# Kernel optimization log

Measured on AMD Instinct MI355X. Metric: run time of the kernel, lower is better.

Reference implementation:

```python
import jax, jax.numpy as jnp
import numpy as np

N = 50000
E = 1600000
INPUT_DIM = 128
HEADS = 4
OUT_DIM = 32
LRELU_ALPHA = 0.2


def setup_inputs() -> dict:
    key = jax.random.key(0)
    k1, k2, k3, k4, k5 = jax.random.split(key, 5)
    gain = 1.0 / (1.0 + LRELU_ALPHA)
    input_proj = jax.random.normal(k1, (N, INPUT_DIM), dtype=jnp.float32)
    edge_index = jax.random.randint(k2, (2, E), 0, N, dtype=jnp.int64)
    W = jax.random.normal(k3, (INPUT_DIM, HEADS * OUT_DIM), dtype=jnp.float32) * (gain / INPUT_DIM) ** 0.5
    A_left = jax.random.normal(k4, (HEADS, OUT_DIM, 1), dtype=jnp.float32) * (gain / OUT_DIM)
    A_right = jax.random.normal(k5, (HEADS, OUT_DIM, 1), dtype=jnp.float32) * (gain / OUT_DIM)
    return {"input_proj": input_proj, "edge_index": edge_index, "W": W, "A_left": A_left, "A_right": A_right}


def reference(input_proj, edge_index, W, A_left, A_right):
    n = input_proj.shape[0]
    heads, out_dim = A_left.shape[0], A_left.shape[1]
    # Linear projection: [N, heads, out_dim]
    H = (input_proj @ W).reshape(n, heads, out_dim)
    # Per-node attention scores: [N, heads]
    H_s = jnp.einsum('nhd,hd->nh', H, A_left[..., 0])
    H_t = jnp.einsum('nhd,hd->nh', H, A_right[..., 0])
    src = edge_index[0]
    tgt = edge_index[1]
    # Edge scores: leaky_relu(H_s[src] + H_t[tgt]) -> [E, heads]
    e = H_s[src] + H_t[tgt]
    e = jnp.where(e > 0, e, LRELU_ALPHA * e)
    # Segment softmax over neighborhoods keyed by source node (global max shift, as in original)
    e = jnp.exp(e - jnp.max(e))
    denom = jax.ops.segment_sum(e, src, num_segments=n)  # [N, heads]
    alpha = e / (denom[src] + 1e-8)
    # Weighted scatter-add aggregation of target features: [N, heads, out_dim]
    msg = alpha[:, :, None] * H[tgt]
    agg = jax.ops.segment_sum(msg, src, num_segments=n)
    # concat_last=True -> [N, heads*out_dim], then ELU
    res = agg.reshape(n, heads * out_dim)
    return jax.nn.elu(res)
```

## Files before the change

### kernel.cpp

```cpp
#include <hip/hip_runtime.h>
#include <hip/hip_fp16.h>

#define DIM 128
#define HEADS 4
#define ODIM 32
#define LRELU 0.2f
#define PT 4096
#define CAP 9216

typedef unsigned int u32;
typedef unsigned short u16;
typedef unsigned char u8;

typedef __attribute__((ext_vector_type(8))) short bf16x8;
typedef __attribute__((ext_vector_type(4))) float f32x4;

__device__ __forceinline__ u16 f2bf(float f) {
    union { u32 u; float f; } x; x.f = f;
    u32 u = x.u;
    u32 r = u + 0x7FFFu + ((u >> 16) & 1u);
    return (u16)(r >> 16);
}
__device__ __forceinline__ u32 pack_h2(float x, float y) {
    union { __half2 h; u32 u; } c;
    c.h = __floats2half2_rn(x, y);
    return c.u;
}
__device__ __forceinline__ float2 up2(u32 b) {
    union { u32 u; __half2 h; } c; c.u = b;
    return __half22float2(c.h);
}

__device__ __forceinline__ int scan256_excl(int v, int t, int* wsum) {
    int lane = t & 63, w = t >> 6;
    int inc = v;
    #pragma unroll
    for (int ofs = 1; ofs < 64; ofs <<= 1) {
        int x = __shfl_up(inc, ofs);
        if (lane >= ofs) inc += x;
    }
    __syncthreads();
    if (lane == 63) wsum[w] = inc;
    __syncthreads();
    int add = 0;
    #pragma unroll
    for (int j = 0; j < 4; ++j) add += (j < w) ? wsum[j] : 0;
    return inc - v + add;
}

__global__ __launch_bounds__(256) void prep_kernel(
    const float* __restrict__ W, u16* __restrict__ Wt, int* __restrict__ bcur)
{
    __shared__ u16 s[128 * 17];
    const int t = threadIdx.x;
    const int b = blockIdx.x;
    if (b == 0) bcur[t] = t * CAP;
    #pragma unroll
    for (int i = 0; i < 8; ++i) {
        int idx = i * 256 + t;
        int kk = idx >> 7;
        int nn = idx & 127;
        s[nn * 17 + kk] = f2bf(W[(b * 16 + kk) * 128 + nn]);
    }
    __syncthreads();
    #pragma unroll
    for (int i = 0; i < 8; ++i) {
        int idx = i * 256 + t;
        int nn = idx >> 4;
        int kk = idx & 15;
        Wt[nn * 128 + b * 16 + kk] = s[nn * 17 + kk];
    }
}

__device__ __forceinline__ void partition_body(
    char* smem, int bid, const int* __restrict__ ei, int* __restrict__ bcur,
    u32* __restrict__ part, int E, int n)
{
    int (*lcnt4)[256] = (int (*)[256])(smem);
    int (*gcur4)[256] = (int (*)[256])(smem + 4096);
    const int t = threadIdx.x;
    const int wv = t >> 6;
    const int base = bid * PT;
    lcnt4[0][t] = 0; lcnt4[1][t] = 0; lcnt4[2][t] = 0; lcnt4[3][t] = 0;
    __syncthreads();

    int srcv[16], tgtv[16];
    #pragma unroll
    for (int i = 0; i < 16; ++i) {
        int e = base + i * 256 + t;
        srcv[i] = (e < E) ? ei[e] : -1;
    }
    #pragma unroll
    for (int i = 0; i < 16; ++i) {
        int e = base + i * 256 + t;
        tgtv[i] = (e < E) ? ei[E + e] : 0;
    }
    u32 key[16];
    int bkt[16];
    #pragma unroll
    for (int i = 0; i < 16; ++i) {
        bkt[i] = -1;
        key[i] = 0;
        if (srcv[i] >= 0) {
            int src = min(srcv[i], n - 1);
            int tgt = max(0, min(tgtv[i], n - 1));
            bkt[i] = src >> 8;
            key[i] = ((u32)(src & 255) << 17) | (u32)tgt;
        }
    }
    #pragma unroll
    for (int i = 0; i < 16; ++i)
        if (bkt[i] >= 0) atomicAdd(&lcnt4[wv][bkt[i]], 1);
    __syncthreads();
    int c0 = lcnt4[0][t], c1 = lcnt4[1][t], c2 = lcnt4[2][t], c3 = lcnt4[3][t];
    int total = c0 + c1 + c2 + c3;
    int gb = (total > 0) ? atomicAdd(&bcur[t], total) : 0;
    gcur4[0][t] = gb;
    gcur4[1][t] = gb + c0;
    gcur4[2][t] = gb + c0 + c1;
    gcur4[3][t] = gb + c0 + c1 + c2;
    __syncthreads();
    #pragma unroll
    for (int i = 0; i < 16; ++i) {
        if (bkt[i] >= 0) {
            int p = atomicAdd(&gcur4[wv][bkt[i]], 1);
            if (p < (bkt[i] + 1) * CAP) part[p] = key[i];
        }
    }
}

__device__ __forceinline__ void proj_body(
    char* smem, int bid, const float* __restrict__ X, const u16* __restrict__ Wt,
    const float* __restrict__ AL, const float* __restrict__ AR,
    u32* __restrict__ Hb, float* __restrict__ Hs, float* __restrict__ Ht, int n)
{
    float* sH  = (float*)smem;
    float* sAL = (float*)(smem + 33792);
    float* sAR = (float*)(smem + 34304);
    const int t = threadIdx.x;
    if (t < DIM) { sAL[t] = AL[t]; sAR[t] = AR[t]; }
    const int row0 = bid * 64;
    const int w = t >> 6, lane = t & 63;
    const int quad = lane >> 4, nIdx = lane & 15;
    const int m = row0 + w * 16 + nIdx;

    f32x4 acc[8];
    #pragma unroll
    for (int c = 0; c < 8; ++c) acc[c] = (f32x4){0.f, 0.f, 0.f, 0.f};

    #pragma unroll
    for (int kq = 0; kq < 4; ++kq) {
        union { bf16x8 v; u16 e[8]; } a;
        if (m < n) {
            const float* xp = &X[(size_t)m * DIM + kq * 32 + quad * 8];
            float4 x0 = *(const float4*)xp;
            float4 x1 = *(const float4*)(xp + 4);
            a.e[0] = f2bf(x0.x); a.e[1] = f2bf(x0.y);
            a.e[2] = f2bf(x0.z); a.e[3] = f2bf(x0.w);
            a.e[4] = f2bf(x1.x); a.e[5] = f2bf(x1.y);
            a.e[6] = f2bf(x1.z); a.e[7] = f2bf(x1.w);
        } else {
            #pragma unroll
            for (int j = 0; j < 8; ++j) a.e[j] = 0;
        }
        #pragma unroll
        for (int c = 0; c < 8; ++c) {
            bf16x8 b = *(const bf16x8*)&Wt[(c * 16 + nIdx) * DIM + kq * 32 + quad * 8];
            acc[c] = __builtin_amdgcn_mfma_f32_16x16x32_bf16(a.v, b, acc[c], 0, 0, 0);
        }
    }
    #pragma unroll
    for (int c = 0; c < 8; ++c)
        #pragma unroll
        for (int r = 0; r < 4; ++r)
            sH[(w * 16 + quad * 4 + r) * 132 + c * 16 + nIdx] = acc[c][r];
    __syncthreads();

    #pragma unroll
    for (int i = 0; i < 16; ++i) {
        int idx = i * 256 + t;
        int r = idx >> 6, d2 = idx & 63;
        int gr = row0 + r;
        if (gr < n) {
            float2 hv = *(const float2*)&sH[r * 132 + 2 * d2];
            Hb[(size_t)gr * 64 + d2] = pack_h2(hv.x, hv.y);
        }
    }
    {
        int r = t >> 2, h = t & 3;
        float s = 0.f, s2 = 0.f;
        #pragma unroll
        for (int q = 0; q < ODIM; q += 4) {
            float4 hv = *(const float4*)&sH[r * 132 + h * ODIM + q];
            s  += hv.x*sAL[h*ODIM+q] + hv.y*sAL[h*ODIM+q+1] + hv.z*sAL[h*ODIM+q+2] + hv.w*sAL[h*ODIM+q+3];
            s2 += hv.x*sAR[h*ODIM+q] + hv.y*sAR[h*ODIM+q+1] + hv.z*sAR[h*ODIM+q+2] + hv.w*sAR[h*ODIM+q+3];
        }
        int gr = row0 + r;
        if (gr < n) { Hs[gr * HEADS + h] = s; Ht[gr * HEADS + h] = s2; }
    }
}

__global__ __launch_bounds__(256) void fused_pp_kernel(
    const float* __restrict__ X, const u16* __restrict__ Wt,
    const float* __restrict__ AL, const float* __restrict__ AR,
    u32* __restrict__ Hb, float* __restrict__ Hs, float* __restrict__ Ht,
    const int* __restrict__ ei, int* __restrict__ bcur, u32* __restrict__ part,
    int n, int E, int partBlocks)
{
    __shared__ alignas(16) char smem[34816];
    if ((int)blockIdx.x < partBlocks)
        partition_body(smem, blockIdx.x, ei, bcur, part, E, n);
    else
        proj_body(smem, blockIdx.x - partBlocks, X, Wt, AL, AR, Hb, Hs, Ht, n);
}

__global__ __launch_bounds__(256) void csrfill_kernel(
    const u32* __restrict__ part, const int* __restrict__ bcur,
    int* __restrict__ off, int* __restrict__ csr_tgt, int n, int ntiles)
{
    __shared__ u32 skey[CAP];
    __shared__ int lc4[4][128];
    __shared__ int lcur4[4][128];
    __shared__ int wsum[4];
    __shared__ int sBase, sCnt;
    const int blk = blockIdx.x, t = threadIdx.x;
    const int b = blk >> 1, half = blk & 1;
    const int wv = t >> 6;
    int myc = (t < ntiles) ? (bcur[t] - t * CAP) : 0;
    myc = max(0, min(myc, CAP));
    int ex = scan256_excl(myc, t, wsum);
    if (t == b) { sBase = ex; sCnt = myc; }
    if (t < 128) { lc4[0][t] = 0; lc4[1][t] = 0; lc4[2][t] = 0; lc4[3][t] = 0; }
    __syncthreads();
    const int pbase = b * CAP;
    const int base = sBase, cnt = sCnt;
    for (int i = t; i < cnt; i += 1024) {
        u32 k[4];
        #pragma unroll
        for (int u = 0; u < 4; ++u) {
            int idx = i + u * 256;
            k[u] = (idx < cnt) ? part[pbase + idx] : 0xFFFFFFFFu;
        }
        #pragma unroll
        for (int u = 0; u < 4; ++u) {
            int idx = i + u * 256;
            if (idx < cnt) skey[idx] = k[u];
            int n8 = (int)(k[u] >> 17);
            if ((n8 >> 7) == half) atomicAdd(&lc4[wv][n8 & 127], 1);
        }
    }
    __syncthreads();
    int c0 = 0, c1 = 0, c2 = 0, c3 = 0, total = 0;
    if (t < 128) {
        c0 = lc4[0][t]; c1 = lc4[1][t]; c2 = lc4[2][t]; c3 = lc4[3][t];
        total = c0 + c1 + c2 + c3;
    }
    int ex2 = scan256_excl(total, t, wsum);
    int halfTot = wsum[0] + wsum[1];
    int myBase = base + (half ? (cnt - halfTot) : 0);
    if (t < 128) {
        lcur4[0][t] = ex2;
        lcur4[1][t] = ex2 + c0;
        lcur4[2][t] = ex2 + c0 + c1;
        lcur4[3][t] = ex2 + c0 + c1 + c2;
        int node = b * 256 + half * 128 + t;
        if (node < n) off[node] = myBase + ex2;
    }
    if (b == ntiles - 1 && half == 0 && t == 0) off[n] = base + cnt;
    __syncthreads();
    for (int i = t; i < cnt; i += 256) {
        u32 key = skey[i];
        int n8 = (int)(key >> 17);
        if ((n8 >> 7) == half) {
            int p = atomicAdd(&lcur4[wv][n8 & 127], 1);
            csr_tgt[myBase + p] = (int)(key & 0x1FFFFu);
        }
    }
}

__global__ __launch_bounds__(256) void agg_kernel(
    const u32* __restrict__ Hb, const float* __restrict__ Hs,
    const float* __restrict__ Ht, const int* __restrict__ off,
    const int* __restrict__ csr_tgt, float2* __restrict__ out, int n, int E)
{
    const int nWaves = gridDim.x * 4;
    const int L = threadIdx.x & 63;
    const int h = L >> 4;
    const int jSel = L >> 2;
    const int hSel = L & 3;

    for (int node = (blockIdx.x * 256 + threadIdx.x) >> 6; node < n;
         node += nWaves) {
        int lo = off[node], hi = off[node + 1];
        lo = max(0, min(lo, E));
        hi = max(lo, min(hi, E));
        if (hi <= lo) {
            out[(size_t)node * 64 + L] = {0.f, 0.f};
            continue;
        }
        float4 hs4 = *(const float4*)&Hs[node * HEADS];
        float hsD = hSel == 0 ? hs4.x : hSel == 1 ? hs4.y : hSel == 2 ? hs4.z : hs4.w;
        float ax = 0.f, ay = 0.f, Sd = 0.f;

        for (int i = lo; i < hi; i += 32) {
            int tl = csr_tgt[min(i + (L & 31), hi - 1)];
            int tA = __shfl(tl, jSel);
            int tB = __shfl(tl, jSel + 16);
            float eA = hsD + Ht[tA * HEADS + hSel];
            float eB = hsD + Ht[tB * HEADS + hSel];
            float wA = (i + jSel < hi)
                           ? __expf(fminf(eA > 0.f ? eA : LRELU * eA, 30.f)) : 0.f;
            float wB = (i + jSel + 16 < hi)
                           ? __expf(fminf(eB > 0.f ? eB : LRELU * eB, 30.f)) : 0.f;
            Sd += wA + wB;
            u32 bb[32];
            #pragma unroll
            for (int j = 0; j < 32; ++j) {
                int sj = __builtin_amdgcn_readlane(tl, j);
                bb[j] = Hb[((size_t)(u32)sj << 6) + L];
            }
            #pragma unroll
            for (int j = 0; j < 16; ++j) {
                float wj = __shfl(wA, (j << 2) | h);
                float2 f = up2(bb[j]);
                ax += wj * f.x;
                ay += wj * f.y;
            }
            #pragma unroll
            for (int j = 0; j < 16; ++j) {
                float wj = __shfl(wB, (j << 2) | h);
                float2 f = up2(bb[j + 16]);
                ax += wj * f.x;
                ay += wj * f.y;
            }
        }
        float S = 0.f;
        #pragma unroll
        for (int j = 0; j < 16; ++j) S += __shfl(Sd, (j << 2) | h);
        float inv = 1.f / (S + 1e-8f);
        float ox = ax * inv, oy = ay * inv;
        ox = ox > 0.f ? ox : (__expf(ox) - 1.f);
        oy = oy > 0.f ? oy : (__expf(oy) - 1.f);
        out[(size_t)node * 64 + L] = {ox, oy};
    }
}

extern "C" void kernel_launch(void* const* d_in, const int* in_sizes, int n_in,
                              void* d_out, int out_size, void* d_ws, size_t ws_size,
                              hipStream_t stream) {
    const float* X  = (const float*)d_in[0];
    const int*   EI = (const int*)d_in[1];
    const float* W  = (const float*)d_in[2];
    const float* AL = (const float*)d_in[3];
    const float* AR = (const float*)d_in[4];
    const int n = in_sizes[0] / DIM;
    const int E = in_sizes[1] / 2;
    const int ntiles = (n + 255) / 256;

    char* ws = (char*)d_ws;
    size_t o = 0;
    auto alloc = [&](size_t bytes) -> void* {
        o = (o + 255) & ~(size_t)255;
        void* p = ws + o;
        o += bytes;
        return p;
    };
    int*   bcur    = (int*)alloc(256 * 4);
    u16*   Wt      = (u16*)alloc((size_t)DIM * DIM * 2);
    int*   off     = (int*)alloc((size_t)(n + 1) * 4);
    float* Hs      = (float*)alloc((size_t)n * HEADS * 4);
    float* Ht      = (float*)alloc((size_t)n * HEADS * 4);
    int*   csr_tgt = (int*)alloc((size_t)E * 4);
    u32*   part    = (u32*)alloc((size_t)ntiles * CAP * 4);
    u32*   Hb      = (u32*)alloc((size_t)n * 64 * 4);

    const int PB = (E + PT - 1) / PT;
    const int JB = (n + 63) / 64;

    prep_kernel<<<8, 256, 0, stream>>>(W, Wt, bcur);
    fused_pp_kernel<<<PB + JB, 256, 0, stream>>>(
        X, Wt, AL, AR, Hb, Hs, Ht, EI, bcur, part, n, E, PB);
    csrfill_kernel<<<ntiles * 2, 256, 0, stream>>>(part, bcur, off, csr_tgt, n, ntiles);
    agg_kernel<<<2048, 256, 0, stream>>>(
        Hb, Hs, Ht, off, csr_tgt, (float2*)d_out, n, E);
}
```

Measured before the change: 196.8 us.

## Replace bucketed partition CSR build with degree histogram, scan, and atomic scatter

Drops the two-level bucket partition and per-tile local sort in favor of a global degree histogram via atomics, a three-kernel prefix scan, and a scatter kernel that places targets with global atomicAdd on per-node cursors. The aggregation kernel also changes from a grid-stride loop to one wave per node with an exact launch size. This removes the fixed-capacity bucket buffer and its overflow risk, but adds several kernel launches, a second full pass over the edge list, and heavy contention on global atomics. Neighbour order inside the CSR becomes nondeterministic.

After: 311.1 us. 58.0% more time.

```diff
diff --git a/kernel.cpp b/kernel.cpp
--- a/kernel.cpp
+++ b/kernel.cpp
@@ -6,7 +6,6 @@
 #define ODIM 32
 #define LRELU 0.2f
 #define PT 4096
-#define CAP 9216
 
 typedef unsigned int u32;
 typedef unsigned short u16;
@@ -49,12 +48,13 @@
 }
 
 __global__ __launch_bounds__(256) void prep_kernel(
-    const float* __restrict__ W, u16* __restrict__ Wt, int* __restrict__ bcur)
+    const float* __restrict__ W, u16* __restrict__ Wt, int* __restrict__ deg,
+    int nPad)
 {
     __shared__ u16 s[128 * 17];
     const int t = threadIdx.x;
     const int b = blockIdx.x;
-    if (b == 0) bcur[t] = t * CAP;
+    for (int i = b * 256 + t; i < nPad; i += 8 * 256) deg[i] = 0;
     #pragma unroll
     for (int i = 0; i < 8; ++i) {
         int idx = i * 256 + t;
@@ -72,19 +72,12 @@
     }
 }
 
-__device__ __forceinline__ void partition_body(
-    char* smem, int bid, const int* __restrict__ ei, int* __restrict__ bcur,
-    u32* __restrict__ part, int E, int n)
-{
-    int (*lcnt4)[256] = (int (*)[256])(smem);
-    int (*gcur4)[256] = (int (*)[256])(smem + 4096);
-    const int t = threadIdx.x;
-    const int wv = t >> 6;
+__device__ __forceinline__ void hist_body(
+    int bid, const int* __restrict__ ei, int* __restrict__ deg, int E, int n)
+{
+    const int t = threadIdx.x;
     const int base = bid * PT;
-    lcnt4[0][t] = 0; lcnt4[1][t] = 0; lcnt4[2][t] = 0; lcnt4[3][t] = 0;
-    __syncthreads();
-
-    int srcv[16], tgtv[16];
+    int srcv[16];
     #pragma unroll
     for (int i = 0; i < 16; ++i) {
         int e = base + i * 256 + t;
@@ -92,39 +85,9 @@
     }
     #pragma unroll
     for (int i = 0; i < 16; ++i) {
-        int e = base + i * 256 + t;
-        tgtv[i] = (e < E) ? ei[E + e] : 0;
-    }
-    u32 key[16];
-    int bkt[16];
-    #pragma unroll
-    for (int i = 0; i < 16; ++i) {
-        bkt[i] = -1;
-        key[i] = 0;
         if (srcv[i] >= 0) {
             int src = min(srcv[i], n - 1);
-            int tgt = max(0, min(tgtv[i], n - 1));
-            bkt[i] = src >> 8;
-            key[i] = ((u32)(src & 255) << 17) | (u32)tgt;
-        }
-    }
-    #pragma unroll
-    for (int i = 0; i < 16; ++i)
-        if (bkt[i] >= 0) atomicAdd(&lcnt4[wv][bkt[i]], 1);
-    __syncthreads();
-    int c0 = lcnt4[0][t], c1 = lcnt4[1][t], c2 = lcnt4[2][t], c3 = lcnt4[3][t];
-    int total = c0 + c1 + c2 + c3;
-    int gb = (total > 0) ? atomicAdd(&bcur[t], total) : 0;
-    gcur4[0][t] = gb;
-    gcur4[1][t] = gb + c0;
-    gcur4[2][t] = gb + c0 + c1;
-    gcur4[3][t] = gb + c0 + c1 + c2;
-    __syncthreads();
-    #pragma unroll
-    for (int i = 0; i < 16; ++i) {
-        if (bkt[i] >= 0) {
-            int p = atomicAdd(&gcur4[wv][bkt[i]], 1);
-            if (p < (bkt[i] + 1) * CAP) part[p] = key[i];
+            atomicAdd(&deg[src], 1);
         }
     }
 }
@@ -200,80 +163,80 @@
     }
 }
 
-__global__ __launch_bounds__(256) void fused_pp_kernel(
+__global__ __launch_bounds__(256) void fused_ph_kernel(
     const float* __restrict__ X, const u16* __restrict__ Wt,
     const float* __restrict__ AL, const float* __restrict__ AR,
     u32* __restrict__ Hb, float* __restrict__ Hs, float* __restrict__ Ht,
-    const int* __restrict__ ei, int* __restrict__ bcur, u32* __restrict__ part,
-    int n, int E, int partBlocks)
+    const int* __restrict__ ei, int* __restrict__ deg,
+    int n, int E, int histBlocks)
 {
     __shared__ alignas(16) char smem[34816];
-    if ((int)blockIdx.x < partBlocks)
-        partition_body(smem, blockIdx.x, ei, bcur, part, E, n);
+    if ((int)blockIdx.x < histBlocks)
+        hist_body(blockIdx.x, ei, deg, E, n);
     else
-        proj_body(smem, blockIdx.x - partBlocks, X, Wt, AL, AR, Hb, Hs, Ht, n);
-}
-
-__global__ __launch_bounds__(256) void csrfill_kernel(
-    const u32* __restrict__ part, const int* __restrict__ bcur,
-    int* __restrict__ off, int* __restrict__ csr_tgt, int n, int ntiles)
-{
-    __shared__ u32 skey[CAP];
-    __shared__ int lc4[4][128];
-    __shared__ int lcur4[4][128];
+        proj_body(smem, blockIdx.x - histBlocks, X, Wt, AL, AR, Hb, Hs, Ht, n);
+}
+
+__global__ __launch_bounds__(256) void scanA_kernel(
+    const int* __restrict__ deg, int* __restrict__ off, int* __restrict__ tsum,
+    int n)
+{
     __shared__ int wsum[4];
-    __shared__ int sBase, sCnt;
-    const int blk = blockIdx.x, t = threadIdx.x;
-    const int b = blk >> 1, half = blk & 1;
-    const int wv = t >> 6;
-    int myc = (t < ntiles) ? (bcur[t] - t * CAP) : 0;
-    myc = max(0, min(myc, CAP));
-    int ex = scan256_excl(myc, t, wsum);
-    if (t == b) { sBase = ex; sCnt = myc; }
-    if (t < 128) { lc4[0][t] = 0; lc4[1][t] = 0; lc4[2][t] = 0; lc4[3][t] = 0; }
-    __syncthreads();
-    const int pbase = b * CAP;
-    const int base = sBase, cnt = sCnt;
-    for (int i = t; i < cnt; i += 1024) {
-        u32 k[4];
-        #pragma unroll
-        for (int u = 0; u < 4; ++u) {
-            int idx = i + u * 256;
-            k[u] = (idx < cnt) ? part[pbase + idx] : 0xFFFFFFFFu;
-        }
-        #pragma unroll
-        for (int u = 0; u < 4; ++u) {
-            int idx = i + u * 256;
-            if (idx < cnt) skey[idx] = k[u];
-            int n8 = (int)(k[u] >> 17);
-            if ((n8 >> 7) == half) atomicAdd(&lc4[wv][n8 & 127], 1);
-        }
-    }
-    __syncthreads();
-    int c0 = 0, c1 = 0, c2 = 0, c3 = 0, total = 0;
-    if (t < 128) {
-        c0 = lc4[0][t]; c1 = lc4[1][t]; c2 = lc4[2][t]; c3 = lc4[3][t];
-        total = c0 + c1 + c2 + c3;
-    }
-    int ex2 = scan256_excl(total, t, wsum);
-    int halfTot = wsum[0] + wsum[1];
-    int myBase = base + (half ? (cnt - halfTot) : 0);
-    if (t < 128) {
-        lcur4[0][t] = ex2;
-        lcur4[1][t] = ex2 + c0;
-        lcur4[2][t] = ex2 + c0 + c1;
-        lcur4[3][t] = ex2 + c0 + c1 + c2;
-        int node = b * 256 + half * 128 + t;
-        if (node < n) off[node] = myBase + ex2;
-    }
-    if (b == ntiles - 1 && half == 0 && t == 0) off[n] = base + cnt;
-    __syncthreads();
-    for (int i = t; i < cnt; i += 256) {
-        u32 key = skey[i];
-        int n8 = (int)(key >> 17);
-        if ((n8 >> 7) == half) {
-            int p = atomicAdd(&lcur4[wv][n8 & 127], 1);
-            csr_tgt[myBase + p] = (int)(key & 0x1FFFFu);
+    const int b = blockIdx.x, t = threadIdx.x;
+    const int node = b * 256 + t;
+    int v = deg[node];
+    int ex = scan256_excl(v, t, wsum);
+    if (node <= n) off[node] = ex;
+    if (t == 255) tsum[b] = ex + v;
+}
+
+__global__ __launch_bounds__(256) void scanB_kernel(
+    const int* __restrict__ tsum, int* __restrict__ toff, int ntiles)
+{
+    __shared__ int wsum[4];
+    const int t = threadIdx.x;
+    int v = (t < ntiles) ? tsum[t] : 0;
+    int ex = scan256_excl(v, t, wsum);
+    if (t < ntiles) toff[t] = ex;
+}
+
+__global__ __launch_bounds__(256) void scanC_kernel(
+    int* __restrict__ off, const int* __restrict__ toff, int* __restrict__ cur,
+    int n)
+{
+    const int b = blockIdx.x, t = threadIdx.x;
+    const int node = b * 256 + t;
+    if (node <= n) {
+        int v = off[node] + toff[b];
+        off[node] = v;
+        if (node < n) cur[node] = v;
+    }
+}
+
+__global__ __launch_bounds__(256) void scatter_kernel(
+    const int* __restrict__ ei, int* __restrict__ cur,
+    int* __restrict__ csr_tgt, int E, int n)
+{
+    const int t = threadIdx.x;
+    const int base = blockIdx.x * PT;
+    int srcv[16], tgtv[16];
+    #pragma unroll
+    for (int i = 0; i < 16; ++i) {
+        int e = base + i * 256 + t;
+        srcv[i] = (e < E) ? ei[e] : -1;
+    }
+    #pragma unroll
+    for (int i = 0; i < 16; ++i) {
+        int e = base + i * 256 + t;
+        tgtv[i] = (e < E) ? ei[E + e] : 0;
+    }
+    #pragma unroll
+    for (int i = 0; i < 16; ++i) {
+        if (srcv[i] >= 0) {
+            int src = min(srcv[i], n - 1);
+            int tgt = max(0, min(tgtv[i], n - 1));
+            int pos = atomicAdd(&cur[src], 1);
+            if (pos >= 0 && pos < E) csr_tgt[pos] = tgt;
         }
     }
 }
@@ -283,66 +246,63 @@
     const float* __restrict__ Ht, const int* __restrict__ off,
     const int* __restrict__ csr_tgt, float2* __restrict__ out, int n, int E)
 {
-    const int nWaves = gridDim.x * 4;
-    const int L = threadIdx.x & 63;
+    int node = (blockIdx.x * 256 + threadIdx.x) >> 6;
+    int L = threadIdx.x & 63;
+    if (node >= n) return;
+    int lo = off[node], hi = off[node + 1];
+    lo = max(0, min(lo, E));
+    hi = max(lo, min(hi, E));
+    if (hi <= lo) {
+        out[(size_t)node * 64 + L] = {0.f, 0.f};
+        return;
+    }
     const int h = L >> 4;
     const int jSel = L >> 2;
     const int hSel = L & 3;
-
-    for (int node = (blockIdx.x * 256 + threadIdx.x) >> 6; node < n;
-         node += nWaves) {
-        int lo = off[node], hi = off[node + 1];
-        lo = max(0, min(lo, E));
-        hi = max(lo, min(hi, E));
-        if (hi <= lo) {
-            out[(size_t)node * 64 + L] = {0.f, 0.f};
-            continue;
-        }
-        float4 hs4 = *(const float4*)&Hs[node * HEADS];
-        float hsD = hSel == 0 ? hs4.x : hSel == 1 ? hs4.y : hSel == 2 ? hs4.z : hs4.w;
-        float ax = 0.f, ay = 0.f, Sd = 0.f;
-
-        for (int i = lo; i < hi; i += 32) {
-            int tl = csr_tgt[min(i + (L & 31), hi - 1)];
-            int tA = __shfl(tl, jSel);
-            int tB = __shfl(tl, jSel + 16);
-            float eA = hsD + Ht[tA * HEADS + hSel];
-            float eB = hsD + Ht[tB * HEADS + hSel];
-            float wA = (i + jSel < hi)
-                           ? __expf(fminf(eA > 0.f ? eA : LRELU * eA, 30.f)) : 0.f;
-            float wB = (i + jSel + 16 < hi)
-                           ? __expf(fminf(eB > 0.f ? eB : LRELU * eB, 30.f)) : 0.f;
-            Sd += wA + wB;
-            u32 bb[32];
-            #pragma unroll
-            for (int j = 0; j < 32; ++j) {
-                int sj = __builtin_amdgcn_readlane(tl, j);
-                bb[j] = Hb[((size_t)(u32)sj << 6) + L];
-            }
-            #pragma unroll
-            for (int j = 0; j < 16; ++j) {
-                float wj = __shfl(wA, (j << 2) | h);
-                float2 f = up2(bb[j]);
-                ax += wj * f.x;
-                ay += wj * f.y;
-            }
-            #pragma unroll
-            for (int j = 0; j < 16; ++j) {
-                float wj = __shfl(wB, (j << 2) | h);
-                float2 f = up2(bb[j + 16]);
-                ax += wj * f.x;
-                ay += wj * f.y;
-            }
-        }
-        float S = 0.f;
-        #pragma unroll
-        for (int j = 0; j < 16; ++j) S += __shfl(Sd, (j << 2) | h);
-        float inv = 1.f / (S + 1e-8f);
-        float ox = ax * inv, oy = ay * inv;
-        ox = ox > 0.f ? ox : (__expf(ox) - 1.f);
-        oy = oy > 0.f ? oy : (__expf(oy) - 1.f);
-        out[(size_t)node * 64 + L] = {ox, oy};
-    }
+    float4 hs4 = *(const float4*)&Hs[node * HEADS];
+    float hsD = hSel == 0 ? hs4.x : hSel == 1 ? hs4.y : hSel == 2 ? hs4.z : hs4.w;
+    float ax = 0.f, ay = 0.f, Sd = 0.f;
+
+    for (int i = lo; i < hi; i += 32) {
+        int tl = csr_tgt[min(i + (L & 31), hi - 1)];
+        int tA = __shfl(tl, jSel);
+        int tB = __shfl(tl, jSel + 16);
+        float eA = hsD + Ht[tA * HEADS + hSel];
+        float eB = hsD + Ht[tB * HEADS + hSel];
+        float wA = (i + jSel < hi)
+                       ? __expf(fminf(eA > 0.f ? eA : LRELU * eA, 30.f)) : 0.f;
+        float wB = (i + jSel + 16 < hi)
+                       ? __expf(fminf(eB > 0.f ? eB : LRELU * eB, 30.f)) : 0.f;
+        Sd += wA + wB;
+        u32 bb[32];
+        #pragma unroll
+        for (int j = 0; j < 32; ++j) {
+            int sj = __builtin_amdgcn_readlane(tl, j);
+            bb[j] = Hb[((size_t)(u32)sj << 6) + L];
+        }
+        #pragma unroll
+        for (int j = 0; j < 16; ++j) {
+            float wj = __shfl(wA, (j << 2) | h);
+            float2 f = up2(bb[j]);
+            ax += wj * f.x;
+            ay += wj * f.y;
+        }
+        #pragma unroll
+        for (int j = 0; j < 16; ++j) {
+            float wj = __shfl(wB, (j << 2) | h);
+            float2 f = up2(bb[j + 16]);
+            ax += wj * f.x;
+            ay += wj * f.y;
+        }
+    }
+    float S = 0.f;
+    #pragma unroll
+    for (int j = 0; j < 16; ++j) S += __shfl(Sd, (j << 2) | h);
+    float inv = 1.f / (S + 1e-8f);
+    float ox = ax * inv, oy = ay * inv;
+    ox = ox > 0.f ? ox : (__expf(ox) - 1.f);
+    oy = oy > 0.f ? oy : (__expf(oy) - 1.f);
+    out[(size_t)node * 64 + L] = {ox, oy};
 }
 
 extern "C" void kernel_launch(void* const* d_in, const int* in_sizes, int n_in,
@@ -356,6 +316,7 @@
     const int n = in_sizes[0] / DIM;
     const int E = in_sizes[1] / 2;
     const int ntiles = (n + 255) / 256;
+    const int nPad = ntiles * 256;
 
     char* ws = (char*)d_ws;
     size_t o = 0;
@@ -365,22 +326,27 @@
         o += bytes;
         return p;
     };
-    int*   bcur    = (int*)alloc(256 * 4);
     u16*   Wt      = (u16*)alloc((size_t)DIM * DIM * 2);
+    int*   deg     = (int*)alloc((size_t)nPad * 4);
     int*   off     = (int*)alloc((size_t)(n + 1) * 4);
+    int*   cur     = (int*)alloc((size_t)nPad * 4);
+    int*   tsum    = (int*)alloc(256 * 4);
+    int*   toff    = (int*)alloc(256 * 4);
     float* Hs      = (float*)alloc((size_t)n * HEADS * 4);
     float* Ht      = (float*)alloc((size_t)n * HEADS * 4);
     int*   csr_tgt = (int*)alloc((size_t)E * 4);
-    u32*   part    = (u32*)alloc((size_t)ntiles * CAP * 4);
     u32*   Hb      = (u32*)alloc((size_t)n * 64 * 4);
 
-    const int PB = (E + PT - 1) / PT;
+    const int HB = (E + PT - 1) / PT;
     const int JB = (n + 63) / 64;
 
-    prep_kernel<<<8, 256, 0, stream>>>(W, Wt, bcur);
-    fused_pp_kernel<<<PB + JB, 256, 0, stream>>>(
-        X, Wt, AL, AR, Hb, Hs, Ht, EI, bcur, part, n, E, PB);
-    csrfill_kernel<<<ntiles * 2, 256, 0, stream>>>(part, bcur, off, csr_tgt, n, ntiles);
-    agg_kernel<<<2048, 256, 0, stream>>>(
+    prep_kernel<<<8, 256, 0, stream>>>(W, Wt, deg, nPad);
+    fused_ph_kernel<<<HB + JB, 256, 0, stream>>>(
+        X, Wt, AL, AR, Hb, Hs, Ht, EI, deg, n, E, HB);
+    scanA_kernel<<<ntiles, 256, 0, stream>>>(deg, off, tsum, n);
+    scanB_kernel<<<1, 256, 0, stream>>>(tsum, toff, ntiles);
+    scanC_kernel<<<ntiles, 256, 0, stream>>>(off, toff, cur, n);
+    scatter_kernel<<<HB, 256, 0, stream>>>(EI, cur, csr_tgt, E, n);
+    agg_kernel<<<(n + 3) / 4, 256, 0, stream>>>(
         Hb, Hs, Ht, off, csr_tgt, (float2*)d_out, n, E);
 }
```
